# Optimization experiments

Measured on AMD Instinct MI355X. Metric: run time of the kernel, lower is better.

## Reference

```python
import jax, jax.numpy as jnp
import numpy as np

D_MODEL = 1024
N_HEAD = 16
D_HEAD = 64
D_CAT = N_HEAD * D_HEAD
HD_MLP = 4096
LN_EPS = 1e-5


def setup_inputs() -> dict:
    key = jax.random.key(0)
    ks = jax.random.split(key, 12)
    bn, t = 2, 2048
    s = lambda fan_in: 1.0 / np.sqrt(fan_in)
    return {
        "x": jax.random.normal(ks[0], (bn, t, D_MODEL), dtype=jnp.float32),
        "mask": jnp.ones((bn, t), dtype=jnp.int32),
        "w_qkv": jax.random.normal(ks[1], (D_MODEL, 3 * D_CAT), dtype=jnp.float32) * s(D_MODEL),
        "w_tail": jax.random.normal(ks[2], (D_CAT, D_MODEL), dtype=jnp.float32) * s(D_CAT),
        "b_tail": jnp.zeros((D_MODEL,), dtype=jnp.float32),
        "ln1_g": jnp.ones((D_MODEL,), dtype=jnp.float32),
        "ln1_b": jnp.zeros((D_MODEL,), dtype=jnp.float32),
        "ln2_g": jnp.ones((D_MODEL,), dtype=jnp.float32),
        "ln2_b": jnp.zeros((D_MODEL,), dtype=jnp.float32),
        "w1": jax.random.normal(ks[3], (D_MODEL, HD_MLP), dtype=jnp.float32) * s(D_MODEL),
        "b1": jnp.zeros((HD_MLP,), dtype=jnp.float32),
        "w2": jax.random.normal(ks[4], (HD_MLP, D_MODEL), dtype=jnp.float32) * s(HD_MLP),
        "b2": jnp.zeros((D_MODEL,), dtype=jnp.float32),
    }


def _layer_norm(x, g, b):
    mu = jnp.mean(x, axis=-1, keepdims=True)
    var = jnp.mean(jnp.square(x - mu), axis=-1, keepdims=True)
    return (x - mu) * jax.lax.rsqrt(var + LN_EPS) * g + b


def _attention(z, mask, w_qkv, w_tail, b_tail):
    bn, t, _ = z.shape
    qkv = z @ w_qkv                      # (bn, t, 3*d_cat)
    qkv = qkv.reshape(bn, t, N_HEAD, 3, D_HEAD)  # chunk layout: per-head [q|k|v]
    q = qkv[..., 0, :].transpose(0, 2, 1, 3)     # (bn, h, t, dh)
    k = qkv[..., 1, :].transpose(0, 2, 1, 3)
    v = qkv[..., 2, :].transpose(0, 2, 1, 3)
    scale = D_HEAD ** -0.5
    dots = jnp.einsum("bhqd,bhkd->bhqk", q, k) * scale
    key_mask = (mask == 0)[:, None, None, :]     # (bn,1,1,t)
    dots = jnp.where(key_mask, -jnp.inf, dots)
    coef = jax.nn.softmax(dots, axis=-1)
    attn = jnp.einsum("bhqk,bhkd->bhqd", coef, v)
    out = attn.transpose(0, 2, 1, 3).reshape(bn, t, D_CAT)
    return out @ w_tail + b_tail


def reference(x, mask, w_qkv, w_tail, b_tail, ln1_g, ln1_b, ln2_g, ln2_b, w1, b1, w2, b2):
    z = _layer_norm(x, ln1_g, ln1_b)
    x = _attention(z, mask, w_qkv, w_tail, b_tail) + x
    z = _layer_norm(x, ln2_g, ln2_b)
    h = jax.nn.gelu(z @ w1 + b1, approximate=False)  # torch GELU default = exact erf
    x = h @ w2 + b2 + x
    return x
```

## Files before the change

### kernel.cpp

```cpp
#include <hip/hip_runtime.h>
#include <hip/hip_bf16.h>

#define DM 1024
#define TT 2048
#define NH 16
#define DH 64
#define HD 4096

typedef __attribute__((ext_vector_type(4))) float f32x4;
typedef __attribute__((ext_vector_type(8))) short s16x8;
typedef __attribute__((ext_vector_type(4))) short s16x4;

static __device__ __forceinline__ short f2bf(float f) {
  __hip_bfloat16 h = __float2bfloat16(f);
  return *reinterpret_cast<short*>(&h);
}

typedef const __attribute__((address_space(1))) char* gas1_t;
typedef __attribute__((address_space(3))) char* las3_t;
static __device__ __forceinline__ void glds16(const void* g, void* l) {
  __builtin_amdgcn_global_load_lds((gas1_t)g, (las3_t)l, 16, 0, 0);
}

__global__ __launch_bounds__(256) void transpose_cvt_k(
    const float* __restrict__ in, short* __restrict__ out, int K, int N)
{
  __shared__ float tile[32][33];
  const int n0 = blockIdx.x * 32, k0 = blockIdx.y * 32;
  const int tx = threadIdx.x & 31, ty = threadIdx.x >> 5;
#pragma unroll
  for (int i = 0; i < 4; ++i)
    tile[ty + i * 8][tx] = in[(size_t)(k0 + ty + i * 8) * N + n0 + tx];
  __syncthreads();
#pragma unroll
  for (int i = 0; i < 4; ++i) {
    int n = ty + i * 8;
    out[(size_t)(n0 + n) * K + k0 + tx] = f2bf(tile[tx][n]);
  }
}

__global__ __launch_bounds__(256) void ln_k(
    const float* __restrict__ x, const float* __restrict__ g,
    const float* __restrict__ b, short* __restrict__ out)
{
  const int row = blockIdx.x;
  const int tid = threadIdx.x;
  const float4 v = ((const float4*)(x + (size_t)row * DM))[tid];
  float s = v.x + v.y + v.z + v.w;
  float q = v.x * v.x + v.y * v.y + v.z * v.z + v.w * v.w;
#pragma unroll
  for (int off = 1; off < 64; off <<= 1) {
    s += __shfl_xor(s, off);
    q += __shfl_xor(q, off);
  }
  __shared__ float ss[4], sq[4];
  const int wave = tid >> 6;
  if ((tid & 63) == 0) { ss[wave] = s; sq[wave] = q; }
  __syncthreads();
  s = ss[0] + ss[1] + ss[2] + ss[3];
  q = sq[0] + sq[1] + sq[2] + sq[3];
  const float mu = s * (1.0f / DM);
  const float var = q * (1.0f / DM) - mu * mu;
  const float rs = rsqrtf(var + 1e-5f);
  const float4 gv = ((const float4*)g)[tid];
  const float4 bv = ((const float4*)b)[tid];
  s16x4 o;
  o[0] = f2bf((v.x - mu) * rs * gv.x + bv.x);
  o[1] = f2bf((v.y - mu) * rs * gv.y + bv.y);
  o[2] = f2bf((v.z - mu) * rs * gv.z + bv.z);
  o[3] = f2bf((v.w - mu) * rs * gv.w + bv.w);
  *(s16x4*)(out + (size_t)row * DM + tid * 4) = o;
}

template<int EPI>
__global__ __launch_bounds__(512, 4) void gemm_pipe(
    const short* __restrict__ A, const short* __restrict__ B,
    const float* __restrict__ bias, const float* __restrict__ res,
    float* __restrict__ outF, short* __restrict__ outB,
    short* __restrict__ outK, short* __restrict__ outV,
    int M, int N, int K)
{
  __shared__ short As[2][2][64 * 64];
  __shared__ short Bs[2][2][64 * 64];
  const int tid = threadIdx.x;
  const int wave = tid >> 6, lane = tid & 63;
  const int l15 = lane & 15, lhi = lane >> 4;
  const int bm = blockIdx.x, bn = blockIdx.y;
  const int wr = wave >> 2;
  const int wc = wave & 3;
  f32x4 acc[4][2] = {};

  const int srow = tid >> 2;
  const int scs = ((tid & 3) ^ ((srow >> 1) & 3)) * 16;
  const int ldst = srow * 64 + (tid & 3) * 16;
  const char* gA = (const char*)(A + (size_t)(bm * 128 + srow) * K);
  const char* gB = (const char*)(B + (size_t)(bn * 128 + srow) * K);

  const int NT = K >> 6;

  auto stagePair = [&](int buf, int kt, int kh) {
    const size_t go = (size_t)kt * 128 + kh * 64 + scs;
    glds16(gA + go, (char*)As[buf][kh] + ldst);
    glds16(gB + go, (char*)Bs[buf][kh] + ldst);
  };

  stagePair(0, 0, 0);
  stagePair(0, 0, 1);

  int buf = 0;
  for (int t = 0; t < NT; ++t) {
#pragma unroll
    for (int kh = 0; kh < 2; ++kh) {
      const bool more = (t + 1 < NT);
      if (more || kh == 0) asm volatile("s_waitcnt vmcnt(2)" ::: "memory");
      else                 asm volatile("s_waitcnt vmcnt(0)" ::: "memory");
      __builtin_amdgcn_s_barrier();
      __builtin_amdgcn_sched_barrier(0);
      s16x8 af[4], bfv[2];
#pragma unroll
      for (int m = 0; m < 4; ++m) {
        const int row = wr * 64 + m * 16 + l15;
        af[m] = *(const s16x8*)((const char*)As[buf][kh] + row * 64 +
                                ((lhi ^ ((row >> 1) & 3)) << 4));
      }
#pragma unroll
      for (int n = 0; n < 2; ++n) {
        const int row = wc * 32 + n * 16 + l15;
        bfv[n] = *(const s16x8*)((const char*)Bs[buf][kh] + row * 64 +
                                 ((lhi ^ ((row >> 1) & 3)) << 4));
      }
      if (more) stagePair(buf ^ 1, t + 1, kh);
      __builtin_amdgcn_s_setprio(1);
#pragma unroll
      for (int m = 0; m < 4; ++m)
#pragma unroll
        for (int n = 0; n < 2; ++n)
          acc[m][n] = __builtin_amdgcn_mfma_f32_16x16x32_bf16(af[m], bfv[n], acc[m][n], 0, 0, 0);
      __builtin_amdgcn_s_setprio(0);
    }
    buf ^= 1;
  }

  const int rowb = bm * 128 + wr * 64;
  const int colb = bn * 128 + wc * 32;
#pragma unroll
  for (int m = 0; m < 4; ++m) {
#pragma unroll
    for (int n = 0; n < 2; ++n) {
      if (EPI == 3) {
        const int col0 = colb + n * 16;
        const int h = col0 / 192;
        const int c0 = col0 - h * 192;
        const int region = c0 >> 6;
        const int d = (c0 & 63) + l15;
        const int row0 = rowb + m * 16 + lhi * 4;
        const int bb = row0 >> 11, tl0 = row0 & 2047;
        const size_t bh = (size_t)bb * NH + h;
        if (region == 2) {
          s16x4 pk;
#pragma unroll
          for (int rr = 0; rr < 4; ++rr) pk[rr] = f2bf(acc[m][n][rr]);
          *(s16x4*)(outV + (bh * 64 + d) * TT + tl0) = pk;
        } else {
          short* dst = (region == 0) ? outB : outK;
          const float qs = (region == 0) ? 0.18033688011112042f : 1.0f;
#pragma unroll
          for (int rr = 0; rr < 4; ++rr)
            dst[(bh * TT + tl0 + rr) * 64 + d] = f2bf(acc[m][n][rr] * qs);
        }
      } else {
        const int col = colb + n * 16 + l15;
        const float bv = bias[col];
#pragma unroll
        for (int rr = 0; rr < 4; ++rr) {
          const int row = rowb + m * 16 + lhi * 4 + rr;
          float v = acc[m][n][rr] + bv;
          if (EPI == 1) {
            v += res[(size_t)row * N + col];
            outF[(size_t)row * N + col] = v;
          } else {
            v = 0.5f * v * (1.0f + erff(v * 0.70710678118f));
            outB[(size_t)row * N + col] = f2bf(v);
          }
        }
      }
    }
  }
}

template<int EPI>
__global__ __launch_bounds__(512, 2) void gemm_pipe_w(
    const short* __restrict__ A, const short* __restrict__ B,
    const float* __restrict__ bias, const float* __restrict__ res,
    float* __restrict__ outF, short* __restrict__ outB,
    int M, int N, int K)
{
  __shared__ short As[2][2][64 * 64];
  __shared__ short Bs[2][2][128 * 64];
  const int tid = threadIdx.x;
  const int wave = tid >> 6, lane = tid & 63;
  const int l15 = lane & 15, lhi = lane >> 4;
  const int bm = blockIdx.x, bn = blockIdx.y;
  const int wr = wave >> 2;
  const int wc = wave & 3;
  f32x4 acc[4][4] = {};

  const int srow = tid >> 2;
  const int scs = ((tid & 3) ^ ((srow >> 1) & 3)) * 16;
  const int ldst = srow * 64 + (tid & 3) * 16;
  const char* gA  = (const char*)(A + (size_t)(bm * 128 + srow) * K);
  const char* gB0 = (const char*)(B + (size_t)(bn * 256 + srow) * K);
  const char* gB1 = gB0 + (size_t)128 * K * 2;

  const int NT = K >> 6;

  auto stageTrip = [&](int buf, int kt, int kh) {
    const size_t go = (size_t)kt * 128 + kh * 64 + scs;
    glds16(gA + go,  (char*)As[buf][kh] + ldst);
    glds16(gB0 + go, (char*)Bs[buf][kh] + ldst);
    glds16(gB1 + go, (char*)Bs[buf][kh] + 8192 + ldst);
  };

  stageTrip(0, 0, 0);
  stageTrip(0, 0, 1);

  int buf = 0;
  for (int t = 0; t < NT; ++t) {
#pragma unroll
    for (int kh = 0; kh < 2; ++kh) {
      const bool more = (t + 1 < NT);
      if (more || kh == 0) asm volatile("s_waitcnt vmcnt(3)" ::: "memory");
      else                 asm volatile("s_waitcnt vmcnt(0)" ::: "memory");
      __builtin_amdgcn_s_barrier();
      __builtin_amdgcn_sched_barrier(0);
      s16x8 af[4], bfv[4];
#pragma unroll
      for (int m = 0; m < 4; ++m) {
        const int row = wr * 64 + m * 16 + l15;
        af[m] = *(const s16x8*)((const char*)As[buf][kh] + row * 64 +
                                ((lhi ^ ((row >> 1) & 3)) << 4));
      }
#pragma unroll
      for (int n = 0; n < 4; ++n) {
        const int row = wc * 64 + n * 16 + l15;
        bfv[n] = *(const s16x8*)((const char*)Bs[buf][kh] + row * 64 +
                                 ((lhi ^ ((row >> 1) & 3)) << 4));
      }
      if (more) stageTrip(buf ^ 1, t + 1, kh);
      __builtin_amdgcn_s_setprio(1);
#pragma unroll
      for (int m = 0; m < 4; ++m)
#pragma unroll
        for (int n = 0; n < 4; ++n)
          acc[m][n] = __builtin_amdgcn_mfma_f32_16x16x32_bf16(af[m], bfv[n], acc[m][n], 0, 0, 0);
      __builtin_amdgcn_s_setprio(0);
    }
    buf ^= 1;
  }

  const int rowb = bm * 128 + wr * 64;
  const int colb = bn * 256 + wc * 64;
#pragma unroll
  for (int m = 0; m < 4; ++m) {
#pragma unroll
    for (int n = 0; n < 4; ++n) {
      const int col = colb + n * 16 + l15;
      const float bv = bias[col];
#pragma unroll
      for (int rr = 0; rr < 4; ++rr) {
        const int row = rowb + m * 16 + lhi * 4 + rr;
        float v = acc[m][n][rr] + bv;
        if (EPI == 1) {
          v += res[(size_t)row * N + col];
          outF[(size_t)row * N + col] = v;
        } else {
          v = 0.5f * v * (1.0f + erff(v * 0.70710678118f));
          outB[(size_t)row * N + col] = f2bf(v);
        }
      }
    }
  }
}

#define PSTRIDE 144
#define PFRAG   2304
__global__ __launch_bounds__(256, 4) void attn_k(
    const short* __restrict__ Qb, const short* __restrict__ Kb,
    const short* __restrict__ Vtb, const int* __restrict__ mask,
    short* __restrict__ outp)
{
  const int tid = threadIdx.x, wave = tid >> 6, lane = tid & 63;
  const int l15 = lane & 15, lhi = lane >> 4;
  const int lb = blockIdx.x;
  const int bh = lb & 31, qb = lb >> 5;
  const int b = bh >> 4, h = bh & 15;
  const int qw = qb * 64 + wave * 16;

  __shared__ short Ks[64 * 64];
  __shared__ short Vt[64 * 64];
  __shared__ char Ps[4 * PFRAG];

  const short* qp = Qb + ((size_t)bh * TT + qw + l15) * 64;
  const s16x8 aq0 = *(const s16x8*)(qp + lhi * 8);
  const s16x8 aq1 = *(const s16x8*)(qp + 32 + lhi * 8);

  f32x4 o[4] = {};
  float mrow = -1e30f, lrow = 0.f;

  const int kr_s = tid >> 2, kc_s = (tid & 3) * 16;
  const int ksw = (kr_s & 7) << 4;

  const short* kgb = Kb + (size_t)bh * TT * 64 + (size_t)kr_s * 64 + kc_s;
  const short* vgb = Vtb + ((size_t)bh * 64 + kr_s) * TT + kc_s;

  s16x8 kpre[2], vpre[2];
  kpre[0] = *(const s16x8*)kgb;       kpre[1] = *(const s16x8*)(kgb + 8);
  vpre[0] = *(const s16x8*)vgb;       vpre[1] = *(const s16x8*)(vgb + 8);
  int m0 = mask[b * TT + lane];

  char* pb = Ps + wave * PFRAG + l15 * PSTRIDE;

  for (int t0 = 0; t0 < TT; t0 += 64) {
    char* krow = (char*)Ks + kr_s * 128;
    *(s16x8*)(krow + ((kc_s * 2) ^ ksw)) = kpre[0];
    *(s16x8*)(krow + ((kc_s * 2 + 16) ^ ksw)) = kpre[1];
    char* vrow = (char*)Vt + kr_s * 128;
    *(s16x8*)(vrow + ((kc_s * 2) ^ ksw)) = vpre[0];
    *(s16x8*)(vrow + ((kc_s * 2 + 16) ^ ksw)) = vpre[1];
    __syncthreads();

    const unsigned long long mb0 = __ballot(m0 != 0);
    const bool full = mb0 == ~0ULL;

    if (t0 + 64 < TT) {
      const short* kg = kgb + (size_t)(t0 + 64) * 64;
      const short* vg = vgb + t0 + 64;
      kpre[0] = *(const s16x8*)kg;  kpre[1] = *(const s16x8*)(kg + 8);
      vpre[0] = *(const s16x8*)vg;  vpre[1] = *(const s16x8*)(vg + 8);
      m0 = mask[b * TT + t0 + 64 + lane];
    }

    f32x4 sv[4];
    __builtin_amdgcn_s_setprio(1);
#pragma unroll
    for (int n = 0; n < 4; ++n) {
      const int row = n * 16 + l15;
      const int sw = (row & 7) << 4;
      const char* kr = (const char*)Ks + row * 128;
      const s16x8 a0 = *(const s16x8*)(kr + ((lhi * 16) ^ sw));
      const s16x8 a1 = *(const s16x8*)(kr + ((64 + lhi * 16) ^ sw));
      f32x4 z = {};
      z = __builtin_amdgcn_mfma_f32_16x16x32_bf16(a0, aq0, z, 0, 0, 0);
      z = __builtin_amdgcn_mfma_f32_16x16x32_bf16(a1, aq1, z, 0, 0, 0);
      sv[n] = z;
    }
    __builtin_amdgcn_s_setprio(0);

    if (!full) {
#pragma unroll
      for (int n = 0; n < 4; ++n) {
        const unsigned nib = (unsigned)(mb0 >> (n * 16 + lhi * 4)) & 0xF;
#pragma unroll
        for (int rr = 0; rr < 4; ++rr)
          if (!((nib >> rr) & 1)) sv[n][rr] = -3e38f;
      }
    }

    float mx0 = fmaxf(sv[0][0], sv[1][0]), mx1 = fmaxf(sv[0][1], sv[1][1]);
    float mx2 = fmaxf(sv[0][2], sv[1][2]), mx3 = fmaxf(sv[0][3], sv[1][3]);
    mx0 = fmaxf(mx0, fmaxf(sv[2][0], sv[3][0]));
    mx1 = fmaxf(mx1, fmaxf(sv[2][1], sv[3][1]));
    mx2 = fmaxf(mx2, fmaxf(sv[2][2], sv[3][2]));
    mx3 = fmaxf(mx3, fmaxf(sv[2][3], sv[3][3]));
    float mx = fmaxf(fmaxf(mx0, mx1), fmaxf(mx2, mx3));
    mx = fmaxf(mx, __shfl_xor(mx, 16));
    mx = fmaxf(mx, __shfl_xor(mx, 32));
    if (__any(mx > mrow + 8.0f)) {
      const float mn = fmaxf(mrow, mx);
      const float alpha = exp2f(mrow - mn);
      mrow = mn;
      lrow *= alpha;
      float ar[4];
#pragma unroll
      for (int rr = 0; rr < 4; ++rr) ar[rr] = __shfl(alpha, lhi * 4 + rr);
#pragma unroll
      for (int db = 0; db < 4; ++db)
#pragma unroll
        for (int rr = 0; rr < 4; ++rr) o[db][rr] *= ar[rr];
    }
    float s0 = 0.f, s1 = 0.f, s2 = 0.f, s3 = 0.f;
#pragma unroll
    for (int n = 0; n < 4; ++n) {
      sv[n][0] = exp2f(sv[n][0] - mrow); s0 += sv[n][0];
      sv[n][1] = exp2f(sv[n][1] - mrow); s1 += sv[n][1];
      sv[n][2] = exp2f(sv[n][2] - mrow); s2 += sv[n][2];
      sv[n][3] = exp2f(sv[n][3] - mrow); s3 += sv[n][3];
    }
    float sum = (s0 + s1) + (s2 + s3);
    sum += __shfl_xor(sum, 16);
    sum += __shfl_xor(sum, 32);
    lrow += sum;

#pragma unroll
    for (int n = 0; n < 4; ++n) {
      s16x4 pk;
#pragma unroll
      for (int rr = 0; rr < 4; ++rr) pk[rr] = f2bf(sv[n][rr]);
      *(s16x4*)(pb + n * 32 + lhi * 8) = pk;
    }
    asm volatile("s_waitcnt lgkmcnt(0)" ::: "memory");
    __builtin_amdgcn_sched_barrier(0);
    s16x8 ap[2];
    ap[0] = *(const s16x8*)(pb + lhi * 16);
    ap[1] = *(const s16x8*)(pb + 64 + lhi * 16);

    __builtin_amdgcn_s_setprio(1);
#pragma unroll
    for (int db = 0; db < 4; ++db) {
      const int d = db * 16 + l15;
      const int swv = (d & 7) << 4;
      const char* vr2 = (const char*)Vt + d * 128;
#pragma unroll
      for (int ks = 0; ks < 2; ++ks) {
        const s16x8 bv = *(const s16x8*)(vr2 + ((ks * 64 + lhi * 16) ^ swv));
        o[db] = __builtin_amdgcn_mfma_f32_16x16x32_bf16(ap[ks], bv, o[db], 0, 0, 0);
      }
    }
    __builtin_amdgcn_s_setprio(0);
    __syncthreads();
  }

  float lr[4];
#pragma unroll
  for (int rr = 0; rr < 4; ++rr) lr[rr] = __shfl(lrow, lhi * 4 + rr);
#pragma unroll
  for (int db = 0; db < 4; ++db) {
#pragma unroll
    for (int rr = 0; rr < 4; ++rr) {
      const int qg = qw + lhi * 4 + rr;
      const int cg = h * 64 + db * 16 + l15;
      outp[(size_t)(b * TT + qg) * DM + cg] = f2bf(o[db][rr] / lr[rr]);
    }
  }
}

extern "C" void kernel_launch(void* const* d_in, const int* in_sizes, int n_in,
                              void* d_out, int out_size, void* d_ws, size_t ws_size,
                              hipStream_t stream)
{
  const float* x      = (const float*)d_in[0];
  const int*   mask   = (const int*)d_in[1];
  const float* w_qkv  = (const float*)d_in[2];
  const float* w_tail = (const float*)d_in[3];
  const float* b_tail = (const float*)d_in[4];
  const float* ln1g   = (const float*)d_in[5];
  const float* ln1b   = (const float*)d_in[6];
  const float* ln2g   = (const float*)d_in[7];
  const float* ln2b   = (const float*)d_in[8];
  const float* w1     = (const float*)d_in[9];
  const float* b1     = (const float*)d_in[10];
  const float* w2     = (const float*)d_in[11];
  const float* b2     = (const float*)d_in[12];

  char* ws = (char*)d_ws;
  size_t off = 0;
  auto take = [&](size_t bytes) {
    char* p = ws + off;
    off += (bytes + 255) & ~(size_t)255;
    return p;
  };
  short* slotW = (short*)take((size_t)4096 * 2048 * 2);
  short* slotZ = (short*)take((size_t)4096 * 1024 * 2);
  short* qb    = (short*)take((size_t)32 * 2048 * 64 * 2);
  short* kb    = (short*)take((size_t)32 * 2048 * 64 * 2);
  short* vtb   = (short*)take((size_t)32 * 64 * 2048 * 2);
  float* x1    = (float*)take((size_t)4096 * 1024 * 4);
  short* hbuf  = (short*)take((size_t)4096 * 4096 * 2);

  transpose_cvt_k<<<dim3(3072 / 32, 1024 / 32), 256, 0, stream>>>(w_qkv, slotW, 1024, 3072);
  ln_k<<<4096, 256, 0, stream>>>(x, ln1g, ln1b, slotZ);
  gemm_pipe<3><<<dim3(32, 24), 512, 0, stream>>>(slotZ, slotW, nullptr, nullptr,
                                                 nullptr, qb, kb, vtb, 4096, 3072, 1024);
  attn_k<<<1024, 256, 0, stream>>>(qb, kb, vtb, mask, slotZ);
  transpose_cvt_k<<<dim3(1024 / 32, 1024 / 32), 256, 0, stream>>>(w_tail, slotW, 1024, 1024);
  gemm_pipe<1><<<dim3(32, 8), 512, 0, stream>>>(slotZ, slotW, b_tail, x,
                                                x1, nullptr, nullptr, nullptr, 4096, 1024, 1024);
  ln_k<<<4096, 256, 0, stream>>>(x1, ln2g, ln2b, slotZ);
  transpose_cvt_k<<<dim3(4096 / 32, 1024 / 32), 256, 0, stream>>>(w1, slotW, 1024, 4096);
  gemm_pipe_w<2><<<dim3(32, 16), 512, 0, stream>>>(slotZ, slotW, b1, nullptr,
                                                   nullptr, hbuf, 4096, 4096, 1024);
  transpose_cvt_k<<<dim3(1024 / 32, 4096 / 32), 256, 0, stream>>>(w2, slotW, 4096, 1024);
  gemm_pipe<1><<<dim3(32, 8), 512, 0, stream>>>(hbuf, slotW, b2, x1,
                                                (float*)d_out, nullptr, nullptr, nullptr, 4096, 1024, 4096);
}
```

Measured before the change: 267.1 us.

## Batch weight transposes into one launch and use 256x256 tiles for MLP up-projection

The four separate weight transpose/convert launches are merged into one kernel that dispatches on block index, with each weight written to its own buffer. This removes launch overhead and lets the conversions run as a single large grid. The GELU up-projection GEMM moves from a 128x256 tile to a 256x256 tile with 8x4 MFMA accumulators per wave, raising arithmetic intensity per LDS load. The cost is more registers and LDS per block and only 256 blocks in the grid, which may leave some CUs idle or limit occupancy.

```diff
diff --git a/kernel.cpp b/kernel.cpp
--- a/kernel.cpp
+++ b/kernel.cpp
@@ -22,11 +22,20 @@
   __builtin_amdgcn_global_load_lds((gas1_t)g, (las3_t)l, 16, 0, 0);
 }
 
-__global__ __launch_bounds__(256) void transpose_cvt_k(
-    const float* __restrict__ in, short* __restrict__ out, int K, int N)
+__global__ __launch_bounds__(256) void transpose_all_k(
+    const float* __restrict__ wqkv, const float* __restrict__ wtail,
+    const float* __restrict__ w1,   const float* __restrict__ w2,
+    short* __restrict__ oqkv, short* __restrict__ otail,
+    short* __restrict__ o1,   short* __restrict__ o2)
 {
   __shared__ float tile[32][33];
-  const int n0 = blockIdx.x * 32, k0 = blockIdx.y * 32;
+  int t = blockIdx.x;
+  const float* in; short* out; int K, N, nx;
+  if (t < 3072)      {          in = wqkv;  out = oqkv;  K = 1024; N = 3072; nx = 96; }
+  else if (t < 4096) { t -= 3072; in = wtail; out = otail; K = 1024; N = 1024; nx = 32; }
+  else if (t < 8192) { t -= 4096; in = w1;    out = o1;    K = 1024; N = 4096; nx = 128; }
+  else               { t -= 8192; in = w2;    out = o2;    K = 4096; N = 1024; nx = 32; }
+  const int n0 = (t % nx) * 32, k0 = (t / nx) * 32;
   const int tx = threadIdx.x & 31, ty = threadIdx.x >> 5;
 #pragma unroll
   for (int i = 0; i < 4; ++i)
@@ -188,14 +197,12 @@
   }
 }
 
-template<int EPI>
-__global__ __launch_bounds__(512, 2) void gemm_pipe_w(
+__global__ __launch_bounds__(512, 2) void gemm_pipe256_gelu(
     const short* __restrict__ A, const short* __restrict__ B,
-    const float* __restrict__ bias, const float* __restrict__ res,
-    float* __restrict__ outF, short* __restrict__ outB,
+    const float* __restrict__ bias, short* __restrict__ outB,
     int M, int N, int K)
 {
-  __shared__ short As[2][2][64 * 64];
+  __shared__ short As[2][2][128 * 64];
   __shared__ short Bs[2][2][128 * 64];
   const int tid = threadIdx.x;
   const int wave = tid >> 6, lane = tid & 63;
@@ -203,40 +210,43 @@
   const int bm = blockIdx.x, bn = blockIdx.y;
   const int wr = wave >> 2;
   const int wc = wave & 3;
-  f32x4 acc[4][4] = {};
+  f32x4 acc[8][4] = {};
 
   const int srow = tid >> 2;
   const int scs = ((tid & 3) ^ ((srow >> 1) & 3)) * 16;
-  const int ldst = srow * 64 + (tid & 3) * 16;
-  const char* gA  = (const char*)(A + (size_t)(bm * 128 + srow) * K);
+  const char* gA0 = (const char*)(A + (size_t)(bm * 256 + srow) * K);
+  const char* gA1 = gA0 + (size_t)128 * K * 2;
   const char* gB0 = (const char*)(B + (size_t)(bn * 256 + srow) * K);
   const char* gB1 = gB0 + (size_t)128 * K * 2;
 
   const int NT = K >> 6;
 
-  auto stageTrip = [&](int buf, int kt, int kh) {
+  auto stageHalf = [&](int buf, int kt, int kh) {
     const size_t go = (size_t)kt * 128 + kh * 64 + scs;
-    glds16(gA + go,  (char*)As[buf][kh] + ldst);
-    glds16(gB0 + go, (char*)Bs[buf][kh] + ldst);
-    glds16(gB1 + go, (char*)Bs[buf][kh] + 8192 + ldst);
+    char* dA = (char*)As[buf][kh] + tid * 16;
+    char* dB = (char*)Bs[buf][kh] + tid * 16;
+    glds16(gA0 + go, dA);
+    glds16(gA1 + go, dA + 8192);
+    glds16(gB0 + go, dB);
+    glds16(gB1 + go, dB + 8192);
   };
 
-  stageTrip(0, 0, 0);
-  stageTrip(0, 0, 1);
+  stageHalf(0, 0, 0);
+  stageHalf(0, 0, 1);
 
   int buf = 0;
   for (int t = 0; t < NT; ++t) {
 #pragma unroll
     for (int kh = 0; kh < 2; ++kh) {
       const bool more = (t + 1 < NT);
-      if (more || kh == 0) asm volatile("s_waitcnt vmcnt(3)" ::: "memory");
+      if (more || kh == 0) asm volatile("s_waitcnt vmcnt(4)" ::: "memory");
       else                 asm volatile("s_waitcnt vmcnt(0)" ::: "memory");
       __builtin_amdgcn_s_barrier();
       __builtin_amdgcn_sched_barrier(0);
-      s16x8 af[4], bfv[4];
-#pragma unroll
-      for (int m = 0; m < 4; ++m) {
-        const int row = wr * 64 + m * 16 + l15;
+      s16x8 af[8], bfv[4];
+#pragma unroll
+      for (int m = 0; m < 8; ++m) {
+        const int row = wr * 128 + m * 16 + l15;
         af[m] = *(const s16x8*)((const char*)As[buf][kh] + row * 64 +
                                 ((lhi ^ ((row >> 1) & 3)) << 4));
       }
@@ -246,10 +256,10 @@
         bfv[n] = *(const s16x8*)((const char*)Bs[buf][kh] + row * 64 +
                                  ((lhi ^ ((row >> 1) & 3)) << 4));
       }
-      if (more) stageTrip(buf ^ 1, t + 1, kh);
+      if (more) stageHalf(buf ^ 1, t + 1, kh);
       __builtin_amdgcn_s_setprio(1);
 #pragma unroll
-      for (int m = 0; m < 4; ++m)
+      for (int m = 0; m < 8; ++m)
 #pragma unroll
         for (int n = 0; n < 4; ++n)
           acc[m][n] = __builtin_amdgcn_mfma_f32_16x16x32_bf16(af[m], bfv[n], acc[m][n], 0, 0, 0);
@@ -258,10 +268,10 @@
     buf ^= 1;
   }
 
-  const int rowb = bm * 128 + wr * 64;
+  const int rowb = bm * 256 + wr * 128;
   const int colb = bn * 256 + wc * 64;
 #pragma unroll
-  for (int m = 0; m < 4; ++m) {
+  for (int m = 0; m < 8; ++m) {
 #pragma unroll
     for (int n = 0; n < 4; ++n) {
       const int col = colb + n * 16 + l15;
@@ -270,13 +280,8 @@
       for (int rr = 0; rr < 4; ++rr) {
         const int row = rowb + m * 16 + lhi * 4 + rr;
         float v = acc[m][n][rr] + bv;
-        if (EPI == 1) {
-          v += res[(size_t)row * N + col];
-          outF[(size_t)row * N + col] = v;
-        } else {
-          v = 0.5f * v * (1.0f + erff(v * 0.70710678118f));
-          outB[(size_t)row * N + col] = f2bf(v);
-        }
+        v = 0.5f * v * (1.0f + erff(v * 0.70710678118f));
+        outB[(size_t)row * N + col] = f2bf(v);
       }
     }
   }
@@ -469,7 +474,10 @@
     off += (bytes + 255) & ~(size_t)255;
     return p;
   };
-  short* slotW = (short*)take((size_t)4096 * 2048 * 2);
+  short* wqkvT = (short*)take((size_t)3072 * 1024 * 2);
+  short* wtailT= (short*)take((size_t)1024 * 1024 * 2);
+  short* w1T   = (short*)take((size_t)4096 * 1024 * 2);
+  short* w2T   = (short*)take((size_t)1024 * 4096 * 2);
   short* slotZ = (short*)take((size_t)4096 * 1024 * 2);
   short* qb    = (short*)take((size_t)32 * 2048 * 64 * 2);
   short* kb    = (short*)take((size_t)32 * 2048 * 64 * 2);
@@ -477,19 +485,17 @@
   float* x1    = (float*)take((size_t)4096 * 1024 * 4);
   short* hbuf  = (short*)take((size_t)4096 * 4096 * 2);
 
-  transpose_cvt_k<<<dim3(3072 / 32, 1024 / 32), 256, 0, stream>>>(w_qkv, slotW, 1024, 3072);
+  transpose_all_k<<<12288, 256, 0, stream>>>(w_qkv, w_tail, w1, w2,
+                                             wqkvT, wtailT, w1T, w2T);
   ln_k<<<4096, 256, 0, stream>>>(x, ln1g, ln1b, slotZ);
-  gemm_pipe<3><<<dim3(32, 24), 512, 0, stream>>>(slotZ, slotW, nullptr, nullptr,
+  gemm_pipe<3><<<dim3(32, 24), 512, 0, stream>>>(slotZ, wqkvT, nullptr, nullptr,
                                                  nullptr, qb, kb, vtb, 4096, 3072, 1024);
   attn_k<<<1024, 256, 0, stream>>>(qb, kb, vtb, mask, slotZ);
-  transpose_cvt_k<<<dim3(1024 / 32, 1024 / 32), 256, 0, stream>>>(w_tail, slotW, 1024, 1024);
-  gemm_pipe<1><<<dim3(32, 8), 512, 0, stream>>>(slotZ, slotW, b_tail, x,
+  gemm_pipe<1><<<dim3(32, 8), 512, 0, stream>>>(slotZ, wtailT, b_tail, x,
                                                 x1, nullptr, nullptr, nullptr, 4096, 1024, 1024);
   ln_k<<<4096, 256, 0, stream>>>(x1, ln2g, ln2b, slotZ);
-  transpose_cvt_k<<<dim3(4096 / 32, 1024 / 32), 256, 0, stream>>>(w1, slotW, 1024, 4096);
-  gemm_pipe_w<2><<<dim3(32, 16), 512, 0, stream>>>(slotZ, slotW, b1, nullptr,
-                                                   nullptr, hbuf, 4096, 4096, 1024);
-  transpose_cvt_k<<<dim3(1024 / 32, 4096 / 32), 256, 0, stream>>>(w2, slotW, 4096, 1024);
-  gemm_pipe<1><<<dim3(32, 8), 512, 0, stream>>>(hbuf, slotW, b2, x1,
+  gemm_pipe256_gelu<<<dim3(16, 16), 512, 0, stream>>>(slotZ, w1T, b1, hbuf,
+                                                      4096, 4096, 1024);
+  gemm_pipe<1><<<dim3(32, 8), 512, 0, stream>>>(hbuf, w2T, b2, x1,
                                                 (float*)d_out, nullptr, nullptr, nullptr, 4096, 1024, 4096);
 }
```

Result: no change. 263.2 us (-1.5%).
